# Optimization experiments

Hardware: AMD Instinct MI355X
Metric: run time of the kernel (lower is better)

Reference implementation:

```python
import jax, jax.numpy as jnp
import numpy as np

B, S, E, H = 4, 2048, 512, 8
DK = E // H  # 64 quantum wires per head


def setup_inputs() -> dict:
    key = jax.random.key(0)
    k1, k2, k3, k4 = jax.random.split(key, 4)
    x = jax.random.normal(k1, (B, S, E), dtype=jnp.float32)
    theta = jax.random.normal(k2, (DK,), dtype=jnp.float32)
    W = jax.random.normal(k3, (E, E), dtype=jnp.float32) * (1.0 / np.sqrt(E))
    b = jax.random.normal(k4, (E,), dtype=jnp.float32) * 0.01
    return {"x": x, "theta": theta, "W": W, "b": b}


def _quantum_project(x, theta):
    # x: [B,S,E] -> heads [B,H,S,DK]. Circuit per wire: RX(x_i) then RX(theta_i),
    # product state => <Z_i> = cos(x_i + theta_i).
    xh = x.reshape(B, S, H, DK).transpose(0, 2, 1, 3)  # [B,H,S,DK]
    return jnp.cos(xh + theta)


def reference(x, theta, W, b):
    q = _quantum_project(x, theta)
    k = _quantum_project(x, theta)
    v = _quantum_project(x, theta)
    scores = jnp.einsum('bhqd,bhkd->bhqk', q, k) / jnp.sqrt(jnp.float32(DK))
    attn = jax.nn.softmax(scores, axis=-1)  # dropout is identity in eval
    out = jnp.einsum('bhqk,bhkd->bhqd', attn, v)  # [B,H,S,DK]
    out = out.transpose(0, 2, 1, 3).reshape(B, S, E)
    return out @ W.T + b
```

## Files before the change

### kernel.cpp

```cpp
#include <hip/hip_runtime.h>
#include <hip/hip_bf16.h>
#include <math.h>

#define B_ 4
#define S_ 2048
#define E_ 512
#define H_ 8
#define DK_ 64

typedef __attribute__((ext_vector_type(8))) short short8;
typedef __attribute__((ext_vector_type(4))) float f32x4;
typedef _Float16 half8 __attribute__((ext_vector_type(8)));
typedef _Float16 half4 __attribute__((ext_vector_type(4)));
typedef __fp16 fp16x2 __attribute__((ext_vector_type(2)));
typedef unsigned uint4v __attribute__((ext_vector_type(4)));

__device__ inline short8 ld8(const void* p) {
  return *reinterpret_cast<const short8*>(p);
}
__device__ inline half8 ld8h(const void* p) {
  return *reinterpret_cast<const half8*>(p);
}

static __device__ inline unsigned pk2(float a, float b) {
  fp16x2 h = __builtin_amdgcn_cvt_pkrtz(a, b);
  return __builtin_bit_cast(unsigned, h);
}
static __device__ inline half8 pack8(float p0, float p1, float p2, float p3,
                                     float p4, float p5, float p6, float p7) {
  uint4v u;
  u[0] = pk2(p0, p1); u[1] = pk2(p2, p3);
  u[2] = pk2(p4, p5); u[3] = pk2(p6, p7);
  return __builtin_bit_cast(half8, u);
}


__global__ __launch_bounds__(256) void prep_g_kernel(
    const float* __restrict__ x, const float* __restrict__ theta,
    _Float16* __restrict__ kA, _Float16* __restrict__ vA) {
  const int bh = blockIdx.y;
  const int b = bh >> 3, h = bh & 7;
  const int s0 = blockIdx.x * 64;
  const int tid = threadIdx.x;
  const int wave = tid >> 6, lane = tid & 63;
  const int col = lane & 15, quad = lane >> 4;
  __shared__ _Float16 tile[64 * 72];

  const float* xp = x + ((size_t)(b * S_ + s0)) * E_ + h * DK_;
#pragma unroll
  for (int it = 0; it < 16; ++it) {
    int idx = it * 256 + tid;
    int sr = idx >> 6, dc = idx & 63;
    tile[sr * 72 + dc] = (_Float16)__cosf(xp[(size_t)sr * E_ + dc] + theta[dc]);
  }
  __syncthreads();

  _Float16* kb = kA + (size_t)bh * (S_ * DK_);
  _Float16* vb = vA + (size_t)bh * (S_ * DK_);
  const int Gbase = s0 >> 5;
#pragma unroll
  for (int it2 = 0; it2 < 2; ++it2) {
    int c = wave + it2 * 4;
    int Gl = c >> 2, g = (c >> 1) & 1, hh = c & 1;
    int ploc = Gl * 32 + ((col >> 2) << 3) + g * 4 + (col & 3);
    half8 v = ld8h(tile + ploc * 72 + hh * 32 + quad * 8);
    *reinterpret_cast<half8*>(
        kb + ((size_t)(Gbase + Gl) * 2048 + (g * 2 + hh) * 512 + lane * 8)) = v;
  }
#pragma unroll
  for (int it2 = 0; it2 < 2; ++it2) {
    int c = wave + it2 * 4;
    int Gl = c >> 2, dcc = c & 3;
    half8 v;
#pragma unroll
    for (int j = 0; j < 8; ++j)
      v[j] = tile[(Gl * 32 + quad * 8 + j) * 72 + dcc * 16 + col];
    *reinterpret_cast<half8*>(
        vb + ((size_t)(Gbase + Gl) * 2048 + dcc * 512 + lane * 8)) = v;
  }
}

__global__ void prep_w_kernel(const float* __restrict__ W, _Float16* __restrict__ wb) {
  int i = (blockIdx.x * 256 + threadIdx.x) * 8;
  float4 a = *reinterpret_cast<const float4*>(W + i);
  float4 c = *reinterpret_cast<const float4*>(W + i + 4);
  half8 v;
  v[0]=(_Float16)a.x; v[1]=(_Float16)a.y; v[2]=(_Float16)a.z; v[3]=(_Float16)a.w;
  v[4]=(_Float16)c.x; v[5]=(_Float16)c.y; v[6]=(_Float16)c.z; v[7]=(_Float16)c.w;
  *reinterpret_cast<half8*>(wb + i) = v;
}

__global__ __launch_bounds__(256, 3) void attn_kernel(
    const _Float16* __restrict__ kA, const _Float16* __restrict__ vA,
    _Float16* __restrict__ ao) {
  const int tid = threadIdx.x;
  const int wave = tid >> 6, lane = tid & 63;
  const int col = lane & 15, quad = lane >> 4;
  const int wg = blockIdx.x + 32 * blockIdx.y;
  const int xcd = wg & 7, slot = wg >> 3;
  const int bh = xcd * 4 + (slot >> 5);
  const int q0 = (slot & 31) * 64;
  const _Float16* kb = kA + (size_t)bh * (S_ * DK_);
  const _Float16* vb = vA + (size_t)bh * (S_ * DK_);

  const _Float16 hC1 = (_Float16)0.18033688011112042f;
  half8 qa[4][2];
#pragma unroll
  for (int qc = 0; qc < 4; ++qc)
#pragma unroll
    for (int hh = 0; hh < 2; ++hh)
      qa[qc][hh] = ld8h(kb + (size_t)((q0 >> 5) + (qc >> 1)) * 2048 +
                        ((qc & 1) * 2 + hh) * 512 + lane * 8) * hC1;

  f32x4 o[4][4];
#pragma unroll
  for (int qc = 0; qc < 4; ++qc)
#pragma unroll
    for (int dc = 0; dc < 4; ++dc) o[qc][dc] = f32x4{0.f, 0.f, 0.f, 0.f};
  float l[4] = {0.f, 0.f, 0.f, 0.f};

  const _Float16* kw = kb + (size_t)wave * 16 * 2048 + lane * 8;
  const _Float16* vw = vb + (size_t)wave * 16 * 2048 + lane * 8;

  for (int it = 0; it < 16; ++it) {
    const _Float16* kit = kw + it * 2048;
    const _Float16* vit = vw + it * 2048;
    half8 kf00 = ld8h(kit);
    half8 kf01 = ld8h(kit + 512);
    half8 kf10 = ld8h(kit + 1024);
    half8 kf11 = ld8h(kit + 1536);
    half8 vf0 = ld8h(vit);
    half8 vf1 = ld8h(vit + 512);
    half8 vf2 = ld8h(vit + 1024);
    half8 vf3 = ld8h(vit + 1536);

    half8 pf[4];
#pragma unroll
    for (int qc = 0; qc < 4; ++qc) {
      f32x4 z0{0.f, 0.f, 0.f, 0.f}, z1{0.f, 0.f, 0.f, 0.f};
      z0 = __builtin_amdgcn_mfma_f32_16x16x32_f16(kf00, qa[qc][0], z0, 0, 0, 0);
      z0 = __builtin_amdgcn_mfma_f32_16x16x32_f16(kf01, qa[qc][1], z0, 0, 0, 0);
      z1 = __builtin_amdgcn_mfma_f32_16x16x32_f16(kf10, qa[qc][0], z1, 0, 0, 0);
      z1 = __builtin_amdgcn_mfma_f32_16x16x32_f16(kf11, qa[qc][1], z1, 0, 0, 0);
      float p0 = __builtin_amdgcn_exp2f(z0[0]);
      float p1 = __builtin_amdgcn_exp2f(z0[1]);
      float p2 = __builtin_amdgcn_exp2f(z0[2]);
      float p3 = __builtin_amdgcn_exp2f(z0[3]);
      float p4 = __builtin_amdgcn_exp2f(z1[0]);
      float p5 = __builtin_amdgcn_exp2f(z1[1]);
      float p6 = __builtin_amdgcn_exp2f(z1[2]);
      float p7 = __builtin_amdgcn_exp2f(z1[3]);
      l[qc] += ((p0 + p1) + (p2 + p3)) + ((p4 + p5) + (p6 + p7));
      pf[qc] = pack8(p0, p1, p2, p3, p4, p5, p6, p7);
    }
#pragma unroll
    for (int qc = 0; qc < 4; ++qc) {
      o[qc][0] = __builtin_amdgcn_mfma_f32_16x16x32_f16(vf0, pf[qc], o[qc][0], 0, 0, 0);
      o[qc][1] = __builtin_amdgcn_mfma_f32_16x16x32_f16(vf1, pf[qc], o[qc][1], 0, 0, 0);
      o[qc][2] = __builtin_amdgcn_mfma_f32_16x16x32_f16(vf2, pf[qc], o[qc][2], 0, 0, 0);
      o[qc][3] = __builtin_amdgcn_mfma_f32_16x16x32_f16(vf3, pf[qc], o[qc][3], 0, 0, 0);
    }
  }

  __shared__ float reds[4096];
#pragma unroll
  for (int qc = 0; qc < 4; ++qc) {
    float t = l[qc];
    t += __shfl_xor(t, 16);
    t += __shfl_xor(t, 32);
    l[qc] = t;
  }
  if (quad == 0) {
#pragma unroll
    for (int qc = 0; qc < 4; ++qc) reds[(wave * 4 + qc) * 16 + col] = l[qc];
  }
  __syncthreads();
  float ltot = 0.f;
#pragma unroll
  for (int w2 = 0; w2 < 4; ++w2) ltot += reds[(w2 * 4 + wave) * 16 + col];
  float inv = __builtin_amdgcn_rcpf(ltot);

  const int b = bh >> 3, h = bh & 7;
  const int qrow = q0 + ((wave >> 1) << 5) + ((col >> 2) << 3) + (wave & 1) * 4 + (col & 3);
  _Float16* op = ao + ((size_t)b * S_ + qrow) * E_ + h * DK_;
#pragma unroll
  for (int qc = 0; qc < 4; ++qc) {
    __syncthreads();
#pragma unroll
    for (int dc = 0; dc < 4; ++dc)
      *reinterpret_cast<f32x4*>(reds + wave * 1024 + lane * 16 + dc * 4) = o[qc][dc];
    __syncthreads();
    if (wave == qc) {
#pragma unroll
      for (int dc = 0; dc < 4; ++dc) {
        f32x4 acc = *reinterpret_cast<const f32x4*>(reds + lane * 16 + dc * 4);
#pragma unroll
        for (int w2 = 1; w2 < 4; ++w2)
          acc = acc + *reinterpret_cast<const f32x4*>(reds + w2 * 1024 + lane * 16 + dc * 4);
        half4 pk4;
        pk4[0] = (_Float16)(acc[0] * inv);
        pk4[1] = (_Float16)(acc[1] * inv);
        pk4[2] = (_Float16)(acc[2] * inv);
        pk4[3] = (_Float16)(acc[3] * inv);
        *reinterpret_cast<half4*>(op + dc * 16 + quad * 4) = pk4;
      }
    }
  }
}

__global__ __launch_bounds__(256) void proj_kernel(
    const _Float16* __restrict__ ao, const _Float16* __restrict__ wb,
    const float* __restrict__ bias, float* __restrict__ out) {
  const int tid = threadIdx.x;
  const int wave = tid >> 6, lane = tid & 63;
  const int col = lane & 15, quad = lane >> 4;
  const int wg = blockIdx.x + 128 * blockIdx.y;
  const int xcd = wg & 7, slot = wg >> 3;
  const int m0 = (xcd * 16 + (slot >> 3)) * 64;
  const int n0 = (slot & 7) * 64;
  __shared__ short at[64 * 136];
  __shared__ short bt[64 * 136];

  const int srw = tid >> 4;
  const int soff = (tid & 15) * 8;

  short8 ap_[4], wp_[4];
#pragma unroll
  for (int it = 0; it < 4; ++it) {
    int row = it * 16 + srw;
    ap_[it] = ld8(ao + (size_t)(m0 + row) * E_ + soff);
    wp_[it] = ld8(wb + (size_t)(n0 + row) * E_ + soff);
  }

  f32x4 acc[4] = {{0.f,0.f,0.f,0.f},{0.f,0.f,0.f,0.f},{0.f,0.f,0.f,0.f},{0.f,0.f,0.f,0.f}};

  for (int k0 = 0; k0 < E_; k0 += 128) {
#pragma unroll
    for (int it = 0; it < 4; ++it) {
      int row = it * 16 + srw;
      *reinterpret_cast<short8*>(at + row * 136 + soff) = ap_[it];
      *reinterpret_cast<short8*>(bt + row * 136 + soff) = wp_[it];
    }
    __syncthreads();
    if (k0 + 128 < E_) {
#pragma unroll
      for (int it = 0; it < 4; ++it) {
        int row = it * 16 + srw;
        ap_[it] = ld8(ao + (size_t)(m0 + row) * E_ + k0 + 128 + soff);
        wp_[it] = ld8(wb + (size_t)(n0 + row) * E_ + k0 + 128 + soff);
      }
    }
#pragma unroll
    for (int ks = 0; ks < 4; ++ks) {
      half8 a = *reinterpret_cast<const half8*>(at + (wave * 16 + col) * 136 + ks * 32 + quad * 8);
#pragma unroll
      for (int f = 0; f < 4; ++f) {
        half8 bb = *reinterpret_cast<const half8*>(bt + (f * 16 + col) * 136 + ks * 32 + quad * 8);
        acc[f] = __builtin_amdgcn_mfma_f32_16x16x32_f16(a, bb, acc[f], 0, 0, 0);
      }
    }
    __syncthreads();
  }

#pragma unroll
  for (int f = 0; f < 4; ++f) {
    float bv = bias[n0 + f * 16 + col];
#pragma unroll
    for (int r = 0; r < 4; ++r) {
      int row = m0 + wave * 16 + quad * 4 + r;
      out[(size_t)row * E_ + n0 + f * 16 + col] = acc[f][r] + bv;
    }
  }
}

extern "C" void kernel_launch(void* const* d_in, const int* in_sizes, int n_in,
                              void* d_out, int out_size, void* d_ws, size_t ws_size,
                              hipStream_t stream) {
  const float* x = (const float*)d_in[0];
  const float* theta = (const float*)d_in[1];
  const float* W = (const float*)d_in[2];
  const float* bias = (const float*)d_in[3];
  float* out = (float*)d_out;
  char* ws = (char*)d_ws;
  const size_t gsz = (size_t)B_ * H_ * S_ * DK_ * 2;
  _Float16* kA = (_Float16*)ws;
  _Float16* vA = (_Float16*)(ws + gsz);
  _Float16* ao = (_Float16*)(ws + 2 * gsz);
  _Float16* wb = (_Float16*)(ws + 3 * gsz);

  prep_g_kernel<<<dim3(S_ / 64, B_ * H_), 256, 0, stream>>>(x, theta, kA, vA);
  prep_w_kernel<<<dim3((E_ * E_) / (256 * 8)), 256, 0, stream>>>(W, wb);
  attn_kernel<<<dim3(S_ / 64, B_ * H_), 256, 0, stream>>>(kA, vA, ao);
  proj_kernel<<<dim3((B_ * S_) / 64, E_ / 64), 256, 0, stream>>>(ao, wb, bias, out);
}
```

Baseline: 125.4 us.

## Merge W conversion into prep kernel, vectorize prep, add MFMA priority, halve epilogue syncs

Folds the fp32-to-fp16 conversion of W into the prep kernel as an extra grid row, removing one kernel launch. The cos/theta prep now uses float4 loads and half4 LDS stores. The attention inner loop raises wave priority around MFMA groups. The output reduction processes two query chunks per pass with a doubled LDS buffer, halving the barriers but raising LDS use, which may reduce occupancy.

New measurement: 123.1 us. Within noise of the previous version (-1.8%).

```diff
diff --git a/kernel.cpp b/kernel.cpp
--- a/kernel.cpp
+++ b/kernel.cpp
@@ -37,21 +37,45 @@
 
 __global__ __launch_bounds__(256) void prep_g_kernel(
     const float* __restrict__ x, const float* __restrict__ theta,
-    _Float16* __restrict__ kA, _Float16* __restrict__ vA) {
+    const float* __restrict__ W, _Float16* __restrict__ kA,
+    _Float16* __restrict__ vA, _Float16* __restrict__ wb) {
+  const int tid = threadIdx.x;
+
+  if (blockIdx.y == B_ * H_) {
+    const int base = (blockIdx.x * 256 + tid) * 8;
+#pragma unroll
+    for (int it = 0; it < 4; ++it) {
+      const int i = base + it * 65536;
+      float4 a = *reinterpret_cast<const float4*>(W + i);
+      float4 c = *reinterpret_cast<const float4*>(W + i + 4);
+      half8 v;
+      v[0]=(_Float16)a.x; v[1]=(_Float16)a.y; v[2]=(_Float16)a.z; v[3]=(_Float16)a.w;
+      v[4]=(_Float16)c.x; v[5]=(_Float16)c.y; v[6]=(_Float16)c.z; v[7]=(_Float16)c.w;
+      *reinterpret_cast<half8*>(wb + i) = v;
+    }
+    return;
+  }
+
   const int bh = blockIdx.y;
   const int b = bh >> 3, h = bh & 7;
   const int s0 = blockIdx.x * 64;
-  const int tid = threadIdx.x;
   const int wave = tid >> 6, lane = tid & 63;
   const int col = lane & 15, quad = lane >> 4;
   __shared__ _Float16 tile[64 * 72];
 
   const float* xp = x + ((size_t)(b * S_ + s0)) * E_ + h * DK_;
-#pragma unroll
-  for (int it = 0; it < 16; ++it) {
-    int idx = it * 256 + tid;
-    int sr = idx >> 6, dc = idx & 63;
-    tile[sr * 72 + dc] = (_Float16)__cosf(xp[(size_t)sr * E_ + dc] + theta[dc]);
+  const int dc4 = (tid & 15) * 4;
+  const float4 th = *reinterpret_cast<const float4*>(theta + dc4);
+#pragma unroll
+  for (int it = 0; it < 4; ++it) {
+    const int sr = it * 16 + (tid >> 4);
+    float4 xv = *reinterpret_cast<const float4*>(xp + (size_t)sr * E_ + dc4);
+    half4 hv;
+    hv[0] = (_Float16)__cosf(xv.x + th.x);
+    hv[1] = (_Float16)__cosf(xv.y + th.y);
+    hv[2] = (_Float16)__cosf(xv.z + th.z);
+    hv[3] = (_Float16)__cosf(xv.w + th.w);
+    *reinterpret_cast<half4*>(tile + sr * 72 + dc4) = hv;
   }
   __syncthreads();
 
@@ -78,16 +102,6 @@
     *reinterpret_cast<half8*>(
         vb + ((size_t)(Gbase + Gl) * 2048 + dcc * 512 + lane * 8)) = v;
   }
-}
-
-__global__ void prep_w_kernel(const float* __restrict__ W, _Float16* __restrict__ wb) {
-  int i = (blockIdx.x * 256 + threadIdx.x) * 8;
-  float4 a = *reinterpret_cast<const float4*>(W + i);
-  float4 c = *reinterpret_cast<const float4*>(W + i + 4);
-  half8 v;
-  v[0]=(_Float16)a.x; v[1]=(_Float16)a.y; v[2]=(_Float16)a.z; v[3]=(_Float16)a.w;
-  v[4]=(_Float16)c.x; v[5]=(_Float16)c.y; v[6]=(_Float16)c.z; v[7]=(_Float16)c.w;
-  *reinterpret_cast<half8*>(wb + i) = v;
 }
 
 __global__ __launch_bounds__(256, 3) void attn_kernel(
@@ -138,10 +152,12 @@
 #pragma unroll
     for (int qc = 0; qc < 4; ++qc) {
       f32x4 z0{0.f, 0.f, 0.f, 0.f}, z1{0.f, 0.f, 0.f, 0.f};
+      __builtin_amdgcn_s_setprio(1);
       z0 = __builtin_amdgcn_mfma_f32_16x16x32_f16(kf00, qa[qc][0], z0, 0, 0, 0);
       z0 = __builtin_amdgcn_mfma_f32_16x16x32_f16(kf01, qa[qc][1], z0, 0, 0, 0);
       z1 = __builtin_amdgcn_mfma_f32_16x16x32_f16(kf10, qa[qc][0], z1, 0, 0, 0);
       z1 = __builtin_amdgcn_mfma_f32_16x16x32_f16(kf11, qa[qc][1], z1, 0, 0, 0);
+      __builtin_amdgcn_s_setprio(0);
       float p0 = __builtin_amdgcn_exp2f(z0[0]);
       float p1 = __builtin_amdgcn_exp2f(z0[1]);
       float p2 = __builtin_amdgcn_exp2f(z0[2]);
@@ -153,6 +169,7 @@
       l[qc] += ((p0 + p1) + (p2 + p3)) + ((p4 + p5) + (p6 + p7));
       pf[qc] = pack8(p0, p1, p2, p3, p4, p5, p6, p7);
     }
+    __builtin_amdgcn_s_setprio(1);
 #pragma unroll
     for (int qc = 0; qc < 4; ++qc) {
       o[qc][0] = __builtin_amdgcn_mfma_f32_16x16x32_f16(vf0, pf[qc], o[qc][0], 0, 0, 0);
@@ -160,9 +177,10 @@
       o[qc][2] = __builtin_amdgcn_mfma_f32_16x16x32_f16(vf2, pf[qc], o[qc][2], 0, 0, 0);
       o[qc][3] = __builtin_amdgcn_mfma_f32_16x16x32_f16(vf3, pf[qc], o[qc][3], 0, 0, 0);
     }
-  }
-
-  __shared__ float reds[4096];
+    __builtin_amdgcn_s_setprio(0);
+  }
+
+  __shared__ float reds[8192];
 #pragma unroll
   for (int qc = 0; qc < 4; ++qc) {
     float t = l[qc];
@@ -183,20 +201,25 @@
   const int b = bh >> 3, h = bh & 7;
   const int qrow = q0 + ((wave >> 1) << 5) + ((col >> 2) << 3) + (wave & 1) * 4 + (col & 3);
   _Float16* op = ao + ((size_t)b * S_ + qrow) * E_ + h * DK_;
-#pragma unroll
-  for (int qc = 0; qc < 4; ++qc) {
+  __syncthreads();
+#pragma unroll
+  for (int qp = 0; qp < 2; ++qp) {
+    if (qp) __syncthreads();
+#pragma unroll
+    for (int hh = 0; hh < 2; ++hh)
+#pragma unroll
+      for (int dc = 0; dc < 4; ++dc)
+        *reinterpret_cast<f32x4*>(reds + hh * 4096 + wave * 1024 + lane * 16 + dc * 4) =
+            o[qp * 2 + hh][dc];
     __syncthreads();
-#pragma unroll
-    for (int dc = 0; dc < 4; ++dc)
-      *reinterpret_cast<f32x4*>(reds + wave * 1024 + lane * 16 + dc * 4) = o[qc][dc];
-    __syncthreads();
-    if (wave == qc) {
+    if ((wave >> 1) == qp) {
+      const float* rp = reds + (wave & 1) * 4096;
 #pragma unroll
       for (int dc = 0; dc < 4; ++dc) {
-        f32x4 acc = *reinterpret_cast<const f32x4*>(reds + lane * 16 + dc * 4);
+        f32x4 acc = *reinterpret_cast<const f32x4*>(rp + lane * 16 + dc * 4);
 #pragma unroll
         for (int w2 = 1; w2 < 4; ++w2)
-          acc = acc + *reinterpret_cast<const f32x4*>(reds + w2 * 1024 + lane * 16 + dc * 4);
+          acc = acc + *reinterpret_cast<const f32x4*>(rp + w2 * 1024 + lane * 16 + dc * 4);
         half4 pk4;
         pk4[0] = (_Float16)(acc[0] * inv);
         pk4[1] = (_Float16)(acc[1] * inv);
@@ -288,8 +311,7 @@
   _Float16* ao = (_Float16*)(ws + 2 * gsz);
   _Float16* wb = (_Float16*)(ws + 3 * gsz);
 
-  prep_g_kernel<<<dim3(S_ / 64, B_ * H_), 256, 0, stream>>>(x, theta, kA, vA);
-  prep_w_kernel<<<dim3((E_ * E_) / (256 * 8)), 256, 0, stream>>>(W, wb);
+  prep_g_kernel<<<dim3(S_ / 64, B_ * H_ + 1), 256, 0, stream>>>(x, theta, W, kA, vA, wb);
   attn_kernel<<<dim3(S_ / 64, B_ * H_), 256, 0, stream>>>(kA, vA, ao);
   proj_kernel<<<dim3((B_ * S_) / 64, E_ / 64), 256, 0, stream>>>(ao, wb, bias, out);
 }
```
